# Kernel optimization log

Hardware: AMD Instinct MI355X
Metric: run time of the kernel (lower is better)

The kernel has to match this reference:

```python
import jax, jax.numpy as jnp
import numpy as np

B, S, D = 16, 512, 2048
NUM_HEADS, NUM_GROUPS = 16, 4
HEAD_DIM = D // NUM_HEADS  # 128
MAX_SEQ_LEN, SHARED_SLOTS = 512, 32
EPS = 1e-6


def _rope_tables(seq_positions):
    # inv_freq over half the head dim, as in the module
    inv_freq = 1.0 / (10000.0 ** (jnp.arange(0, HEAD_DIM, 2, dtype=jnp.float32) / HEAD_DIM))
    freqs = jnp.outer(seq_positions.astype(jnp.float32), inv_freq)  # [S, HEAD_DIM//2]
    return jnp.cos(freqs), jnp.sin(freqs)


def _apply_rope(x, cos, sin):
    # x: [b, s, h, head_dim]; cos/sin: [s, 1, head_dim//2] (broadcast over heads)
    x1, x2 = jnp.split(x, 2, axis=-1)
    real = x1 * cos - x2 * sin
    imag = x1 * sin + x2 * cos
    return jnp.concatenate([real, imag], axis=-1).astype(x.dtype)


def _rmsnorm(x, scale):
    # flax RMSNorm with dtype=float32: compute in fp32
    x = x.astype(jnp.float32)
    ms = jnp.mean(jnp.square(x), axis=-1, keepdims=True)
    return x * jax.lax.rsqrt(ms + EPS) * scale


def setup_inputs() -> dict:
    key = jax.random.key(0)
    ks = jax.random.split(key, 10)
    w = 0.02
    return {
        "x": jax.random.normal(ks[0], (B, S, D), dtype=jnp.float32),
        "wq": jax.random.normal(ks[1], (D, D), dtype=jnp.float32) * w,
        "bq": jnp.zeros((D,), dtype=jnp.float32),
        "wk": jax.random.normal(ks[2], (D, NUM_GROUPS * HEAD_DIM), dtype=jnp.float32) * w,
        "bk": jnp.zeros((NUM_GROUPS * HEAD_DIM,), dtype=jnp.float32),
        "wv": jax.random.normal(ks[3], (D, NUM_GROUPS * HEAD_DIM), dtype=jnp.float32) * w,
        "bv": jnp.zeros((NUM_GROUPS * HEAD_DIM,), dtype=jnp.float32),
        "wo": jax.random.normal(ks[4], (D, D), dtype=jnp.float32) * w,
        "bo": jnp.zeros((D,), dtype=jnp.float32),
        "q_norm_scale": jnp.ones((HEAD_DIM,), dtype=jnp.float32),
        "k_norm_scale": jnp.ones((HEAD_DIM,), dtype=jnp.float32),
    }


def reference(x, wq, bq, wk, bk, wv, bv, wo, bo, q_norm_scale, k_norm_scale):
    b, s, d = x.shape
    rep = NUM_HEADS // NUM_GROUPS
    head_scale = HEAD_DIM ** (-0.5)  # applied once explicitly by the module

    # nnx.Linear(dtype=float16): projections computed in fp16
    xh = x.astype(jnp.float16)
    q = (xh @ wq.astype(jnp.float16) + bq.astype(jnp.float16)).reshape(b, s, NUM_HEADS, HEAD_DIM)
    k = (xh @ wk.astype(jnp.float16) + bk.astype(jnp.float16)).reshape(b, s, NUM_GROUPS, HEAD_DIM)
    v = (xh @ wv.astype(jnp.float16) + bv.astype(jnp.float16)).reshape(b, s, NUM_GROUPS, HEAD_DIM)

    # QK RMSNorm (fp32)
    q = _rmsnorm(q, q_norm_scale)
    k = _rmsnorm(k, k_norm_scale)

    # RoPE (default positions 0..s-1)
    pos = jnp.arange(s)
    cos, sin = _rope_tables(pos)
    cos = cos[:, None, :]
    sin = sin[:, None, :]
    q = _apply_rope(q, cos, sin) * head_scale
    k = _apply_rope(k, cos, sin)

    q = q.astype(jnp.float16)
    k = k.astype(jnp.float16)
    v = v.astype(jnp.float16)

    # GQA without materializing repeated k/v: [b, s, groups, rep, head_dim]
    qg = q.reshape(b, s, NUM_GROUPS, rep, HEAD_DIM)
    # dot_product_attention applies its own 1/sqrt(head_dim) (double-scale, faithful)
    logits = jnp.einsum('btgrh,bsgh->bgrts', qg, k,
                        preferred_element_type=jnp.float32) * head_scale

    causal = pos[:, None] >= pos[None, :]  # [s, s]
    logits = jnp.where(causal[None, None, None, :, :], logits, jnp.finfo(jnp.float32).min)
    probs = jax.nn.softmax(logits, axis=-1).astype(jnp.float16)

    out = jnp.einsum('bgrts,bsgh->btgrh', probs, v)  # [b, s, groups, rep, head_dim]
    out = out.reshape(b, s, d)
    return out @ wo.astype(jnp.float16) + bo.astype(jnp.float16)
```

## Files before the change

kernel.cpp:

```cpp
#include <hip/hip_runtime.h>

#define NB 16
#define NS 512
#define ND 2048
#define NH 16
#define NG 4
#define NHD 128
#define NM (NB * NS)
#define NKD (NG * NHD)
#define NKV 1024
#define HEAD_SCALE 0.08838834764831845f

typedef _Float16 h8 __attribute__((ext_vector_type(8)));
typedef float fx4 __attribute__((ext_vector_type(4)));

__device__ __forceinline__ void gload16(const void* g, void* l) {
  __builtin_amdgcn_global_load_lds(
      (__attribute__((address_space(1))) void*)(unsigned long long)g,
      (__attribute__((address_space(3))) void*)(unsigned long long)l,
      16, 0, 0);
}


__global__ void prep_kernel(const float* __restrict__ x, _Float16* __restrict__ xh,
                            const float* __restrict__ wq, _Float16* __restrict__ wqt,
                            const float* __restrict__ wk, const float* __restrict__ wv,
                            _Float16* __restrict__ wkvt,
                            const float* __restrict__ wo, _Float16* __restrict__ wot,
                            float* __restrict__ cosT, float* __restrict__ sinT,
                            const float* __restrict__ bk, const float* __restrict__ bv,
                            float* __restrict__ bkv) {
  __shared__ float t[64][65];
  const int bid = blockIdx.x, tid = threadIdx.x;
  if (bid < 2048) {
    const fx4* p = (const fx4*)x;
    h8* o = (h8*)xh;
#pragma unroll
    for (int it = 0; it < 4; ++it) {
      int i = (it * 2048 + bid) * 256 + tid;
      fx4 a = p[2 * i], b = p[2 * i + 1];
      h8 hv;
      hv[0] = (_Float16)a[0]; hv[1] = (_Float16)a[1]; hv[2] = (_Float16)a[2]; hv[3] = (_Float16)a[3];
      hv[4] = (_Float16)b[0]; hv[5] = (_Float16)b[1]; hv[6] = (_Float16)b[2]; hv[7] = (_Float16)b[3];
      o[i] = hv;
    }
    return;
  }
  int lb = bid - 2048;
  const float* src;
  _Float16* dst;
  int K, N;
  if (lb < 1024)      { src = wq; dst = wqt; K = ND; N = ND; }
  else if (lb < 1280) { lb -= 1024; src = wk; dst = wkvt; K = ND; N = NKD; }
  else if (lb < 1536) { lb -= 1280; src = wv; dst = wkvt + (size_t)NKD * ND; K = ND; N = NKD; }
  else if (lb < 2560) { lb -= 1536; src = wo; dst = wot; K = ND; N = ND; }
  else if (lb < 2688) {
    int i = (lb - 2560) * 256 + tid;
    int s = i >> 6, f = i & 63;
    float inv = exp2f(-(float)f * (13.287712379549449f / 64.0f));
    float a = (float)s * inv;
    cosT[i] = cosf(a);
    sinT[i] = sinf(a);
    return;
  } else {
#pragma unroll
    for (int it = 0; it < 4; ++it) {
      int idx = it * 256 + tid;
      bkv[idx] = (idx < NKD) ? bk[idx] : bv[idx - NKD];
    }
    return;
  }
  const int ntil = N >> 6;
  const int n0 = (lb % ntil) * 64, k0 = (lb / ntil) * 64;
#pragma unroll
  for (int it = 0; it < 16; ++it) {
    int idx = it * 256 + tid;
    int r = idx >> 6, c = idx & 63;
    t[r][c] = src[(size_t)(k0 + r) * N + n0 + c];
  }
  __syncthreads();
#pragma unroll
  for (int it = 0; it < 16; ++it) {
    int idx = it * 256 + tid;
    int r = idx >> 6, c = idx & 63;
    dst[(size_t)(n0 + r) * K + k0 + c] = (_Float16)t[c][r];
  }
}

__global__ void vtrans_kernel(const _Float16* __restrict__ kv, _Float16* __restrict__ vt) {
  __shared__ _Float16 t[64][72];
  int st = blockIdx.x, dt = blockIdx.y, bg = blockIdx.z;
  int b = bg >> 2, g = bg & 3;
  const _Float16* src = kv + ((size_t)(b * NS + st * 64)) * NKV + NKD + g * NHD + dt * 64;
#pragma unroll
  for (int it = 0; it < 2; ++it) {
    int idx = it * 256 + threadIdx.x;
    int r = idx >> 3, c = (idx & 7) * 8;
    *(h8*)&t[r][c] = *(const h8*)(src + (size_t)r * NKV + c);
  }
  __syncthreads();
  _Float16* dst = vt + ((size_t)bg * NHD + dt * 64) * NS + st * 64;
#pragma unroll
  for (int it = 0; it < 2; ++it) {
    int idx = it * 256 + threadIdx.x;
    int r = idx >> 3, c = (idx & 7) * 8;
    h8 o;
#pragma unroll
    for (int e = 0; e < 8; ++e) o[e] = t[c + e][r];
    *(h8*)(dst + (size_t)r * NS + c) = o;
  }
}

__global__ void norm_rope_kernel(_Float16* __restrict__ X, const float* __restrict__ scale,
                                 const float* __restrict__ cosT, const float* __restrict__ sinT,
                                 int hshift, int rowStride, float outScale) {
  int wid = threadIdx.x >> 6, lane = threadIdx.x & 63;
  int task = blockIdx.x * 4 + wid;
  int row = task >> hshift;
  int head = task & ((1 << hshift) - 1);
  _Float16* p = X + (size_t)row * rowStride + head * NHD;
  float x1 = (float)p[lane], x2 = (float)p[lane + 64];
  float ss = x1 * x1 + x2 * x2;
#pragma unroll
  for (int m = 1; m < 64; m <<= 1) ss += __shfl_xor(ss, m, 64);
  float rn = rsqrtf(ss * (1.0f / 128.0f) + 1e-6f);
  int s = row & (NS - 1);
  float c = cosT[s * 64 + lane], sn = sinT[s * 64 + lane];
  float n1 = x1 * rn * scale[lane], n2 = x2 * rn * scale[64 + lane];
  p[lane] = (_Float16)((n1 * c - n2 * sn) * outScale);
  p[lane + 64] = (_Float16)((n1 * sn + n2 * c) * outScale);
}

__device__ __forceinline__ void st_out(float* p, float v) { *p = v; }
__device__ __forceinline__ void st_out(_Float16* p, float v) { *p = (_Float16)v; }


template <typename OT>
__global__ __launch_bounds__(256, 3) void gemm_bt_kernel(
    const _Float16* __restrict__ A, const _Float16* __restrict__ Bt,
    const float* __restrict__ bias, OT* __restrict__ C, int N, int K) {
  __shared__ alignas(16) _Float16 As[128 * 64];
  __shared__ alignas(16) _Float16 Bs[128 * 64];
  const int tid = threadIdx.x;
  const int lane = tid & 63, wid = tid >> 6;
  const int wr = wid >> 1, wc = wid & 1;
  const int la = lane & 15, lb = (lane >> 4) * 8;
  const int bm = blockIdx.y * 128, bn = blockIdx.x * 128;

  fx4 acc[4][4] = {};

  for (int kt = 0; kt < K; kt += 64) {
    const _Float16* Ag = A + (size_t)bm * K + kt;
    const _Float16* Bg = Bt + (size_t)bn * K + kt;
#pragma unroll
    for (int it = 0; it < 4; ++it) {
      int cb = it * 256 + wid * 64;
      int ca = cb + lane;
      int r = ca >> 3, cc = ca & 7;
      gload16(Ag + (size_t)r * K + cc * 8, &As[cb * 8]);
      gload16(Bg + (size_t)r * K + cc * 8, &Bs[cb * 8]);
    }
    __syncthreads();
#pragma unroll
    for (int kk = 0; kk < 2; ++kk) {
      h8 af[4], bf[4];
#pragma unroll
      for (int m = 0; m < 4; ++m)
        af[m] = *(const h8*)&As[(wr * 64 + m * 16 + la) * 64 + kk * 32 + lb];
#pragma unroll
      for (int n = 0; n < 4; ++n)
        bf[n] = *(const h8*)&Bs[(wc * 64 + n * 16 + la) * 64 + kk * 32 + lb];
#pragma unroll
      for (int m = 0; m < 4; ++m)
#pragma unroll
        for (int n = 0; n < 4; ++n)
          acc[m][n] = __builtin_amdgcn_mfma_f32_16x16x32_f16(af[m], bf[n], acc[m][n], 0, 0, 0);
    }
    __syncthreads();
  }
#pragma unroll
  for (int m = 0; m < 4; ++m) {
    int row0 = bm + wr * 64 + m * 16 + (lane >> 4) * 4;
#pragma unroll
    for (int n = 0; n < 4; ++n) {
      int col = bn + wc * 64 + n * 16 + la;
      float bvv = bias[col];
#pragma unroll
      for (int r = 0; r < 4; ++r)
        st_out(&C[(size_t)(row0 + r) * N + col], acc[m][n][r] + bvv);
    }
  }
}


template <typename OT>
__global__ __launch_bounds__(512, 2) void gemm256_kernel(
    const _Float16* __restrict__ A, const _Float16* __restrict__ Bt,
    const float* __restrict__ bias, OT* __restrict__ C, int N, int K) {
  __shared__ alignas(16) _Float16 As[2][2][256 * 32];
  __shared__ alignas(16) _Float16 Bs[2][2][256 * 32];
  const int tid = threadIdx.x;
  const int lane = tid & 63, w = tid >> 6;
  const int wr = w >> 2, wc = w & 3;
  const int la = lane & 15, lq = lane >> 4;
  const int lin = (blockIdx.x & 7) * 32 + (blockIdx.x >> 3);
  const int nbx = N >> 8;
  const int by = lin / nbx, bx = lin % nbx;
  const int bm = by * 256, bn = bx * 256;
  const int NT = K >> 6;

  fx4 acc[8][4] = {};

  {
    const _Float16* Ag = A + (size_t)bm * K;
    const _Float16* Bg = Bt + (size_t)bn * K;
#pragma unroll
    for (int sh = 0; sh < 2; ++sh) {
#pragma unroll
      for (int i = 0; i < 2; ++i) {
        int cb = i * 512 + w * 64;
        int s = cb + lane;
        int r = s >> 2, c = s & 3;
        gload16(Ag + (size_t)r * K + sh * 32 + ((c ^ ((r >> 1) & 3)) << 3), &As[0][sh][cb * 8]);
      }
#pragma unroll
      for (int i = 0; i < 2; ++i) {
        int cb = i * 512 + w * 64;
        int s = cb + lane;
        int r = s >> 2, c = s & 3;
        gload16(Bg + (size_t)r * K + sh * 32 + ((c ^ ((r >> 1) & 3)) << 3), &Bs[0][sh][cb * 8]);
      }
    }
  }
  asm volatile("s_waitcnt vmcnt(4)" ::: "memory");
  __builtin_amdgcn_s_barrier();

  for (int kt = 0; kt < NT; ++kt) {
    const int cur = kt & 1;
    const int nxt = cur ^ 1;
    const bool more = (kt + 1 < NT);
    const _Float16* Ag = A + (size_t)bm * K + (kt + 1) * 64;
    const _Float16* Bg = Bt + (size_t)bn * K + (kt + 1) * 64;
    h8 bf[4];
#pragma unroll
    for (int ph = 0; ph < 4; ++ph) {
      const int kh = ph >> 1, g = ph & 1;
      h8 af[4];
#pragma unroll
      for (int mi = 0; mi < 4; ++mi) {
        int row = wr * 128 + (g * 4 + mi) * 16 + la;
        af[mi] = *(const h8*)&As[cur][kh][row * 32 + ((lq ^ ((row >> 1) & 3)) << 3)];
      }
      if (g == 0) {
#pragma unroll
        for (int ni = 0; ni < 4; ++ni) {
          int row = wc * 64 + ni * 16 + la;
          bf[ni] = *(const h8*)&Bs[cur][kh][row * 32 + ((lq ^ ((row >> 1) & 3)) << 3)];
        }
      }
      if (more) {
        const int sh = ph >> 1;
        const _Float16* Sg = (ph & 1) ? Bg : Ag;
        _Float16* Ld = (ph & 1) ? &Bs[nxt][sh][0] : &As[nxt][sh][0];
#pragma unroll
        for (int i = 0; i < 2; ++i) {
          int cb = i * 512 + w * 64;
          int s = cb + lane;
          int r = s >> 2, c = s & 3;
          gload16(Sg + (size_t)r * K + sh * 32 + ((c ^ ((r >> 1) & 3)) << 3), Ld + cb * 8);
        }
      }
      if (ph == 1 || ph == 3) {
        if (more) asm volatile("s_waitcnt vmcnt(4)" ::: "memory");
        else      asm volatile("s_waitcnt vmcnt(0)" ::: "memory");
      }
      __builtin_amdgcn_s_barrier();
      asm volatile("s_waitcnt lgkmcnt(0)" ::: "memory");
      __builtin_amdgcn_sched_barrier(0);
      __builtin_amdgcn_s_setprio(1);
#pragma unroll
      for (int mi = 0; mi < 4; ++mi)
#pragma unroll
        for (int ni = 0; ni < 4; ++ni)
          acc[g * 4 + mi][ni] = __builtin_amdgcn_mfma_f32_16x16x32_f16(
              af[mi], bf[ni], acc[g * 4 + mi][ni], 0, 0, 0);
      __builtin_amdgcn_s_setprio(0);
      __builtin_amdgcn_sched_barrier(0);
      __builtin_amdgcn_s_barrier();
    }
  }
#pragma unroll
  for (int mi = 0; mi < 8; ++mi) {
    int row0 = bm + wr * 128 + mi * 16 + lq * 4;
#pragma unroll
    for (int ni = 0; ni < 4; ++ni) {
      int col = bn + wc * 64 + ni * 16 + la;
      float bvv = bias[col];
#pragma unroll
      for (int r = 0; r < 4; ++r)
        st_out(&C[(size_t)(row0 + r) * N + col], acc[mi][ni][r] + bvv);
    }
  }
}


__global__ __launch_bounds__(512, 4) void attn_kernel(
    const _Float16* __restrict__ Q, const _Float16* __restrict__ KV,
    const _Float16* __restrict__ Vt, _Float16* __restrict__ ctx,
    const float* __restrict__ qns, const float* __restrict__ cosT,
    const float* __restrict__ sinT) {
  __shared__ alignas(16) _Float16 Ks[2][64 * 128];
  __shared__ alignas(16) _Float16 Vs[2][128 * 64];
  __shared__ alignas(16) _Float16 Ps[8][16 * 64];

  const int bid = blockIdx.x;
  const int logical = (bid & 7) * 64 + (bid >> 3);
  const int b = logical >> 5;
  const int g = (logical >> 3) & 3;
  const int jp = logical & 7;
  const int j1 = jp, j2 = 15 - jp;

  const int tid = threadIdx.x;
  const int lane = tid & 63, w = tid >> 6;
  const int la = lane & 15, lq = lane >> 4;
  const int h = g * 4 + (w & 3);
  const int rh = w >> 2;

  const _Float16* Vg = Vt + (size_t)(b * NG + g) * NHD * NS;

  auto stage = [&](int buf, int kt) {
    const _Float16* Kg = KV + ((size_t)(b * NS + kt * 64)) * NKV + g * NHD;
#pragma unroll
    for (int it = 0; it < 2; ++it) {
      int cb = it * 512 + w * 64;
      int s = cb + lane;
      int rr = s >> 4, c = s & 15;
      gload16(Kg + (size_t)rr * NKV + ((c ^ (rr & 7)) * 8), &Ks[buf][cb * 8]);
    }
#pragma unroll
    for (int it = 0; it < 2; ++it) {
      int cb = it * 512 + w * 64;
      int s = cb + lane;
      int rr = s >> 3, c = s & 7;
      gload16(Vg + (size_t)rr * NS + kt * 64 + ((c ^ (rr & 7)) * 8), &Vs[buf][cb * 8]);
    }
  };

  const int nt1 = ((j1 * 32 + 31) >> 6) + 1;
  const int nt2 = ((j2 * 32 + 31) >> 6) + 1;
  const int ntotal = nt1 + nt2;

  h8 qf[4];
  fx4 oacc[8];
  float mrun[4], lrun[4];

  stage(0, 0);
  int cur = 0;
  for (int t = 0; t < ntotal; ++t) {
    const bool inA = t < nt1;
    const int j = inA ? j1 : j2;
    const int kt = inA ? t : t - nt1;
    const int ntj = inA ? nt1 : nt2;
    __syncthreads();
    if (t + 1 < ntotal) {
      int nkt = (t + 1 < nt1) ? (t + 1) : (t + 1 - nt1);
      stage(cur ^ 1, nkt);
    }
    if (kt == 0) {
      const int qrow = j * 32 + rh * 16 + la;
      const _Float16* Qg = Q + ((size_t)(b * NS + qrow)) * ND + h * NHD + lq * 8;
      float xq[4][8];
      float ss = 0.f;
#pragma unroll
      for (int kc = 0; kc < 4; ++kc) {
        h8 v = *(const h8*)(Qg + kc * 32);
#pragma unroll
        for (int e = 0; e < 8; ++e) { xq[kc][e] = (float)v[e]; ss += xq[kc][e] * xq[kc][e]; }
      }
      ss += __shfl_xor(ss, 16, 64);
      ss += __shfl_xor(ss, 32, 64);
      float rn = rsqrtf(ss * (1.0f / 128.0f) + 1e-6f);
#pragma unroll
      for (int kc = 0; kc < 2; ++kc) {
        const float* s1p = qns + kc * 32 + lq * 8;
        const float* s2p = qns + (kc + 2) * 32 + lq * 8;
        const float* ctp = cosT + qrow * 64 + kc * 32 + lq * 8;
        const float* stp = sinT + qrow * 64 + kc * 32 + lq * 8;
        fx4 s1a = *(const fx4*)s1p, s1b = *(const fx4*)(s1p + 4);
        fx4 s2a = *(const fx4*)s2p, s2b = *(const fx4*)(s2p + 4);
        fx4 ca = *(const fx4*)ctp, cb2 = *(const fx4*)(ctp + 4);
        fx4 sa = *(const fx4*)stp, sb = *(const fx4*)(stp + 4);
#pragma unroll
        for (int e = 0; e < 8; ++e) {
          float sc1 = (e < 4) ? s1a[e & 3] : s1b[e & 3];
          float sc2 = (e < 4) ? s2a[e & 3] : s2b[e & 3];
          float cc = (e < 4) ? ca[e & 3] : cb2[e & 3];
          float sn = (e < 4) ? sa[e & 3] : sb[e & 3];
          float n1 = xq[kc][e] * rn * sc1;
          float n2 = xq[kc + 2][e] * rn * sc2;
          qf[kc][e] = (_Float16)((n1 * cc - n2 * sn) * HEAD_SCALE);
          qf[kc + 2][e] = (_Float16)((n1 * sn + n2 * cc) * HEAD_SCALE);
        }
      }
#pragma unroll
      for (int f = 0; f < 8; ++f) oacc[f] = fx4{0.f, 0.f, 0.f, 0.f};
#pragma unroll
      for (int r = 0; r < 4; ++r) { mrun[r] = -1e30f; lrun[r] = 0.f; }
    }

    fx4 sc[4] = {};
    __builtin_amdgcn_s_setprio(1);
#pragma unroll
    for (int n = 0; n < 4; ++n) {
      int row = n * 16 + la;
#pragma unroll
      for (int kc = 0; kc < 4; ++kc) {
        h8 bk = *(const h8*)&Ks[cur][row * 128 + (((kc * 4 + lq) ^ (la & 7)) * 8)];
        sc[n] = __builtin_amdgcn_mfma_f32_16x16x32_f16(qf[kc], bk, sc[n], 0, 0, 0);
      }
    }
    __builtin_amdgcn_s_setprio(0);

    const int qrow0 = j * 32 + rh * 16 + lq * 4;
    const bool maskT = (kt == ntj - 1);
    float pv[4][4];
    float rm[4] = {-1e30f, -1e30f, -1e30f, -1e30f};
#pragma unroll
    for (int n = 0; n < 4; ++n) {
      int kv = kt * 64 + n * 16 + la;
#pragma unroll
      for (int r = 0; r < 4; ++r) {
        float sv = sc[n][r] * HEAD_SCALE;
        sv = (maskT && kv > qrow0 + r) ? -1e30f : sv;
        pv[n][r] = sv;
        rm[r] = fmaxf(rm[r], sv);
      }
    }
#pragma unroll
    for (int r = 0; r < 4; ++r) {
#pragma unroll
      for (int m = 1; m < 16; m <<= 1) rm[r] = fmaxf(rm[r], __shfl_xor(rm[r], m, 64));
      float mn = fmaxf(mrun[r], rm[r]);
      float corr = __expf(mrun[r] - mn);
      mrun[r] = mn;
      lrun[r] *= corr;
#pragma unroll
      for (int f = 0; f < 8; ++f) oacc[f][r] *= corr;
    }
    float rs[4] = {0.f, 0.f, 0.f, 0.f};
#pragma unroll
    for (int n = 0; n < 4; ++n)
#pragma unroll
      for (int r = 0; r < 4; ++r) {
        float e = __expf(pv[n][r] - mrun[r]);
        pv[n][r] = e;
        rs[r] += e;
      }
#pragma unroll
    for (int r = 0; r < 4; ++r) {
#pragma unroll
      for (int m = 1; m < 16; m <<= 1) rs[r] += __shfl_xor(rs[r], m, 64);
      lrun[r] += rs[r];
    }

#pragma unroll
    for (int n = 0; n < 4; ++n)
#pragma unroll
      for (int r = 0; r < 4; ++r) {
        int row = lq * 4 + r;
        int chsw = (n * 2 + (la >> 3)) ^ (row & 7);
        Ps[w][row * 64 + chsw * 8 + (la & 7)] = (_Float16)pv[n][r];
      }
    asm volatile("s_waitcnt lgkmcnt(0)" ::: "memory");
    __builtin_amdgcn_sched_barrier(0);
    h8 pf[2];
#pragma unroll
    for (int ks = 0; ks < 2; ++ks)
      pf[ks] = *(const h8*)&Ps[w][la * 64 + (((ks * 4 + lq) ^ (la & 7)) * 8)];

    __builtin_amdgcn_s_setprio(1);
#pragma unroll
    for (int f = 0; f < 8; ++f) {
      int row = f * 16 + la;
#pragma unroll
      for (int ks = 0; ks < 2; ++ks) {
        h8 bv = *(const h8*)&Vs[cur][row * 64 + (((ks * 4 + lq) ^ (la & 7)) * 8)];
        oacc[f] = __builtin_amdgcn_mfma_f32_16x16x32_f16(pf[ks], bv, oacc[f], 0, 0, 0);
      }
    }
    __builtin_amdgcn_s_setprio(0);

    if (maskT) {
      _Float16* Cg = ctx + ((size_t)(b * NS + qrow0)) * ND + h * NHD + la;
      float inv_l[4];
#pragma unroll
      for (int r = 0; r < 4; ++r) inv_l[r] = 1.0f / lrun[r];
#pragma unroll
      for (int f = 0; f < 8; ++f)
#pragma unroll
        for (int r = 0; r < 4; ++r)
          Cg[(size_t)r * ND + f * 16] = (_Float16)(oacc[f][r] * inv_l[r]);
    }
    cur ^= 1;
  }
}


extern "C" void kernel_launch(void* const* d_in, const int* in_sizes, int n_in,
                              void* d_out, int out_size, void* d_ws, size_t ws_size,
                              hipStream_t stream) {
  (void)in_sizes; (void)n_in; (void)out_size; (void)ws_size;
  const float* x = (const float*)d_in[0];
  const float* wq = (const float*)d_in[1];
  const float* bq = (const float*)d_in[2];
  const float* wk = (const float*)d_in[3];
  const float* bk = (const float*)d_in[4];
  const float* wv = (const float*)d_in[5];
  const float* bv = (const float*)d_in[6];
  const float* wo = (const float*)d_in[7];
  const float* bo = (const float*)d_in[8];
  const float* qns = (const float*)d_in[9];
  const float* kns = (const float*)d_in[10];

  char* ws = (char*)d_ws;
  size_t off = 0;
  _Float16* xh = (_Float16*)(ws + off); off += (size_t)NM * ND * 2;
  _Float16* wqt = (_Float16*)(ws + off); off += (size_t)ND * ND * 2;
  _Float16* wkvt = (_Float16*)(ws + off); off += (size_t)NKV * ND * 2;
  _Float16* wot = (_Float16*)(ws + off); off += (size_t)ND * ND * 2;
  _Float16* Qb = (_Float16*)(ws + off); off += (size_t)NM * ND * 2;
  _Float16* KVbuf = (_Float16*)(ws + off); off += (size_t)NM * NKV * 2;
  float* cosT = (float*)(ws + off); off += (size_t)NS * 64 * 4;
  float* sinT = (float*)(ws + off); off += (size_t)NS * 64 * 4;
  float* bkv = (float*)(ws + off); off += (size_t)NKV * 4;
  _Float16* ctx = xh;
  _Float16* Vtg = wqt;

  prep_kernel<<<dim3(4737), 256, 0, stream>>>(x, xh, wq, wqt, wk, wv, wkvt, wo, wot,
                                              cosT, sinT, bk, bv, bkv);

  gemm256_kernel<_Float16><<<dim3(256), dim3(512), 0, stream>>>(xh, wqt, bq, Qb, ND, ND);
  gemm_bt_kernel<_Float16><<<dim3(NKV / 128, NM / 128), 256, 0, stream>>>(xh, wkvt, bkv, KVbuf, NKV, ND);

  norm_rope_kernel<<<dim3(NM * NG / 4), 256, 0, stream>>>(KVbuf, kns, cosT, sinT, 2, NKV, 1.0f);

  vtrans_kernel<<<dim3(NS / 64, NHD / 64, NB * NG), 256, 0, stream>>>(KVbuf, Vtg);

  attn_kernel<<<dim3(512), dim3(512), 0, stream>>>(Qb, KVbuf, Vtg, ctx, qns, cosT, sinT);

  gemm256_kernel<float><<<dim3(256), dim3(512), 0, stream>>>(ctx, wot, bo, (float*)d_out, ND, ND);
}
```

Measured before the change: 297.7 us.

## Merge K norm/rope and V transpose launches; stage attention output through LDS

Combines the K RMSNorm+RoPE kernel and the V transpose kernel into one launch. Block indices below 8192 do norm/rope and the rest do the transpose, which removes one kernel launch and the gap between them. The attention epilogue now writes the normalized output tile into the per-wave LDS P buffer and reads it back as 16-byte vectors. That replaces scattered 2-byte global stores with coalesced ones, at the cost of extra LDS traffic and waitcnt stalls.

```diff
diff --git a/kernel.cpp b/kernel.cpp
--- a/kernel.cpp
+++ b/kernel.cpp
@@ -87,14 +87,37 @@
   }
 }
 
-__global__ void vtrans_kernel(const _Float16* __restrict__ kv, _Float16* __restrict__ vt) {
+
+__global__ void kv_post_kernel(_Float16* __restrict__ kv, _Float16* __restrict__ vt,
+                               const float* __restrict__ kns,
+                               const float* __restrict__ cosT, const float* __restrict__ sinT) {
   __shared__ _Float16 t[64][72];
-  int st = blockIdx.x, dt = blockIdx.y, bg = blockIdx.z;
-  int b = bg >> 2, g = bg & 3;
+  const int bid = blockIdx.x, tid = threadIdx.x;
+  if (bid < 8192) {
+    int wid = tid >> 6, lane = tid & 63;
+    int task = bid * 4 + wid;
+    int row = task >> 2;
+    int head = task & 3;
+    _Float16* p = kv + (size_t)row * NKV + head * NHD;
+    float x1 = (float)p[lane], x2 = (float)p[lane + 64];
+    float ss = x1 * x1 + x2 * x2;
+#pragma unroll
+    for (int m = 1; m < 64; m <<= 1) ss += __shfl_xor(ss, m, 64);
+    float rn = rsqrtf(ss * (1.0f / 128.0f) + 1e-6f);
+    int s = row & (NS - 1);
+    float c = cosT[s * 64 + lane], sn = sinT[s * 64 + lane];
+    float n1 = x1 * rn * kns[lane], n2 = x2 * rn * kns[64 + lane];
+    p[lane] = (_Float16)(n1 * c - n2 * sn);
+    p[lane + 64] = (_Float16)(n1 * sn + n2 * c);
+    return;
+  }
+  const int v = bid - 8192;
+  const int st = v & 7, dt = (v >> 3) & 1, bg = v >> 4;
+  const int b = bg >> 2, g = bg & 3;
   const _Float16* src = kv + ((size_t)(b * NS + st * 64)) * NKV + NKD + g * NHD + dt * 64;
 #pragma unroll
   for (int it = 0; it < 2; ++it) {
-    int idx = it * 256 + threadIdx.x;
+    int idx = it * 256 + tid;
     int r = idx >> 3, c = (idx & 7) * 8;
     *(h8*)&t[r][c] = *(const h8*)(src + (size_t)r * NKV + c);
   }
@@ -102,33 +125,13 @@
   _Float16* dst = vt + ((size_t)bg * NHD + dt * 64) * NS + st * 64;
 #pragma unroll
   for (int it = 0; it < 2; ++it) {
-    int idx = it * 256 + threadIdx.x;
+    int idx = it * 256 + tid;
     int r = idx >> 3, c = (idx & 7) * 8;
     h8 o;
 #pragma unroll
     for (int e = 0; e < 8; ++e) o[e] = t[c + e][r];
     *(h8*)(dst + (size_t)r * NS + c) = o;
   }
-}
-
-__global__ void norm_rope_kernel(_Float16* __restrict__ X, const float* __restrict__ scale,
-                                 const float* __restrict__ cosT, const float* __restrict__ sinT,
-                                 int hshift, int rowStride, float outScale) {
-  int wid = threadIdx.x >> 6, lane = threadIdx.x & 63;
-  int task = blockIdx.x * 4 + wid;
-  int row = task >> hshift;
-  int head = task & ((1 << hshift) - 1);
-  _Float16* p = X + (size_t)row * rowStride + head * NHD;
-  float x1 = (float)p[lane], x2 = (float)p[lane + 64];
-  float ss = x1 * x1 + x2 * x2;
-#pragma unroll
-  for (int m = 1; m < 64; m <<= 1) ss += __shfl_xor(ss, m, 64);
-  float rn = rsqrtf(ss * (1.0f / 128.0f) + 1e-6f);
-  int s = row & (NS - 1);
-  float c = cosT[s * 64 + lane], sn = sinT[s * 64 + lane];
-  float n1 = x1 * rn * scale[lane], n2 = x2 * rn * scale[64 + lane];
-  p[lane] = (_Float16)((n1 * c - n2 * sn) * outScale);
-  p[lane + 64] = (_Float16)((n1 * sn + n2 * c) * outScale);
 }
 
 __device__ __forceinline__ void st_out(float* p, float v) { *p = v; }
@@ -491,15 +494,31 @@
     __builtin_amdgcn_s_setprio(0);
 
     if (maskT) {
-      _Float16* Cg = ctx + ((size_t)(b * NS + qrow0)) * ND + h * NHD + la;
       float inv_l[4];
 #pragma unroll
       for (int r = 0; r < 4; ++r) inv_l[r] = 1.0f / lrun[r];
-#pragma unroll
-      for (int f = 0; f < 8; ++f)
-#pragma unroll
-        for (int r = 0; r < 4; ++r)
-          Cg[(size_t)r * ND + f * 16] = (_Float16)(oacc[f][r] * inv_l[r]);
+      _Float16* base = ctx + ((size_t)(b * NS + j * 32 + rh * 16)) * ND + h * NHD;
+      _Float16* Pw = &Ps[w][0];
+#pragma unroll
+      for (int p = 0; p < 2; ++p) {
+        if ((lq >> 1) == p) {
+          int relrow = (lq & 1) * 4;
+#pragma unroll
+          for (int f = 0; f < 8; ++f)
+#pragma unroll
+            for (int r = 0; r < 4; ++r)
+              Pw[(relrow + r) * 128 + f * 16 + la] = (_Float16)(oacc[f][r] * inv_l[r]);
+        }
+        asm volatile("s_waitcnt lgkmcnt(0)" ::: "memory");
+        __builtin_amdgcn_sched_barrier(0);
+        int rr = lane >> 3, d0 = (lane & 7) * 16;
+        h8 v0 = *(const h8*)&Pw[rr * 128 + d0];
+        h8 v1 = *(const h8*)&Pw[rr * 128 + d0 + 8];
+        asm volatile("s_waitcnt lgkmcnt(0)" ::: "memory");
+        __builtin_amdgcn_sched_barrier(0);
+        *(h8*)&base[(size_t)(p * 8 + rr) * ND + d0] = v0;
+        *(h8*)&base[(size_t)(p * 8 + rr) * ND + d0 + 8] = v1;
+      }
     }
     cur ^= 1;
   }
@@ -542,9 +561,7 @@
   gemm256_kernel<_Float16><<<dim3(256), dim3(512), 0, stream>>>(xh, wqt, bq, Qb, ND, ND);
   gemm_bt_kernel<_Float16><<<dim3(NKV / 128, NM / 128), 256, 0, stream>>>(xh, wkvt, bkv, KVbuf, NKV, ND);
 
-  norm_rope_kernel<<<dim3(NM * NG / 4), 256, 0, stream>>>(KVbuf, kns, cosT, sinT, 2, NKV, 1.0f);
-
-  vtrans_kernel<<<dim3(NS / 64, NHD / 64, NB * NG), 256, 0, stream>>>(KVbuf, Vtg);
+  kv_post_kernel<<<dim3(9216), 256, 0, stream>>>(KVbuf, Vtg, kns, cosT, sinT);
 
   attn_kernel<<<dim3(512), dim3(512), 0, stream>>>(Qb, KVbuf, Vtg, ctx, qns, cosT, sinT);
 
```

Result: no change. 303.6 us (+2.0%).
